# Kernel tuning notes

Measured on AMD Instinct MI355X. Metric: run time of the kernel, lower is better.

## Reference

```python
import jax, jax.numpy as jnp
import numpy as np

I = 1024
H = 1024
B = 4096
EPS = 1e-5

def layer_norm(x, gamma, beta):
    mu = jnp.mean(x, axis=-1, keepdims=True)
    var = jnp.var(x, axis=-1, keepdims=True)
    return (x - mu) * jax.lax.rsqrt(var + EPS) * gamma + beta

def setup_inputs() -> dict:
    key = jax.random.key(0)
    ks = jax.random.split(key, 5)
    return {
        "input": jax.random.normal(ks[0], (B, I), dtype=jnp.float32),
        "hx": jax.random.normal(ks[1], (B, H), dtype=jnp.float32),
        "cx": jax.random.normal(ks[2], (B, H), dtype=jnp.float32),
        "weight_ih": jax.random.normal(ks[3], (4 * H, I), dtype=jnp.float32),
        "weight_hh": jax.random.normal(ks[4], (4 * H, H), dtype=jnp.float32),
        "gamma_i": jnp.ones((4 * H,), jnp.float32),
        "beta_i": jnp.zeros((4 * H,), jnp.float32),
        "gamma_h": jnp.ones((4 * H,), jnp.float32),
        "beta_h": jnp.zeros((4 * H,), jnp.float32),
        "gamma_c": jnp.ones((H,), jnp.float32),
        "beta_c": jnp.zeros((H,), jnp.float32),
    }

def reference(input, hx, cx, weight_ih, weight_hh,
              gamma_i, beta_i, gamma_h, beta_h, gamma_c, beta_c):
    # igates: [B, 4H]
    igates = layer_norm(jnp.dot(input, weight_ih.T), gamma_i, beta_i)
    hgates = layer_norm(jnp.dot(hx, weight_hh.T), gamma_h, beta_h)
    gates = igates + hgates
    ingate, forgetgate, cellgate, outgate = jnp.split(gates, 4, axis=1)
    ingate = jax.nn.sigmoid(ingate)
    forgetgate = jax.nn.sigmoid(forgetgate)
    cellgate = jnp.tanh(cellgate)
    outgate = jax.nn.sigmoid(outgate)
    cy = layer_norm(forgetgate * cx + ingate * cellgate, gamma_c, beta_c)
    hy = outgate * jnp.tanh(cy)
    return (hy, hy, cy)
```

## Files before the change

kernel.cpp:

```cpp
#include <hip/hip_runtime.h>

#define EPS 1e-5f

typedef unsigned short u16;
typedef __attribute__((ext_vector_type(8))) __bf16 bf16x8;
typedef __attribute__((ext_vector_type(4))) float f32x4;
typedef __attribute__((ext_vector_type(8))) unsigned short ushort8;

__device__ inline float bf2f(u16 h) {
  union { unsigned u; float f; } x; x.u = ((unsigned)h) << 16; return x.f;
}
__device__ inline u16 f2bf(float f) {
  union { float f; unsigned u; } x; x.f = f;
  unsigned r = x.u + 0x7fffu + ((x.u >> 16) & 1u);
  return (u16)(r >> 16);
}
__device__ inline float sigmoidf(float x) { return 1.0f / (1.0f + __expf(-x)); }

__global__ __launch_bounds__(256) void cast4_f32_bf16(
    const float* __restrict__ s0, const float* __restrict__ s1,
    const float* __restrict__ s2, const float* __restrict__ s3,
    u16* __restrict__ d0, u16* __restrict__ d1,
    u16* __restrict__ d2, u16* __restrict__ d3, int n)
{
  const float* s = (blockIdx.y == 0) ? s0 : (blockIdx.y == 1) ? s1 : (blockIdx.y == 2) ? s2 : s3;
  u16*         d = (blockIdx.y == 0) ? d0 : (blockIdx.y == 1) ? d1 : (blockIdx.y == 2) ? d2 : d3;
  int i = (blockIdx.x * 256 + threadIdx.x) * 8;
  if (i >= n) return;
  float4 a = *(const float4*)(s + i);
  float4 b = *(const float4*)(s + i + 4);
  ushort8 o;
  o[0] = f2bf(a.x); o[1] = f2bf(a.y); o[2] = f2bf(a.z); o[3] = f2bf(a.w);
  o[4] = f2bf(b.x); o[5] = f2bf(b.y); o[6] = f2bf(b.z); o[7] = f2bf(b.w);
  *(ushort8*)(d + i) = o;
}

#define MFMA_ __builtin_amdgcn_mfma_f32_16x16x32_bf16

#define STAGE_A(nx, k0) { _Pragma("unroll") for (int i_ = 0; i_ < 4; ++i_) \
  __builtin_amdgcn_global_load_lds( \
      (const __attribute__((address_space(1))) void*)(gA + (size_t)(i_ * 64) * K + (k0)), \
      (__attribute__((address_space(3))) void*)(&sA[nx][(i_ * 512 + (w << 6)) * 8]), 16, 0, 0); }
#define STAGE_B(nx, k0) { _Pragma("unroll") for (int i_ = 0; i_ < 4; ++i_) \
  __builtin_amdgcn_global_load_lds( \
      (const __attribute__((address_space(1))) void*)(gB + (size_t)(i_ * 64) * K + (k0)), \
      (__attribute__((address_space(3))) void*)(&sB[nx][(i_ * 512 + (w << 6)) * 8]), 16, 0, 0); }

#define LDA(mi, sl) (*(const bf16x8*)&sa[(arow + (mi) * 16) * 64 + (sl)])
#define LDB(ni, sl) (*(const bf16x8*)&sb[(brow + (ni) * 16) * 64 + (sl)])

#define PHASE(m0, sl, RB) { \
  bf16x8 a0 = LDA(m0 + 0, sl), a1 = LDA(m0 + 1, sl), a2 = LDA(m0 + 2, sl), a3 = LDA(m0 + 3, sl); \
  if (RB) { q0 = LDB(0, sl); q1 = LDB(1, sl); q2 = LDB(2, sl); q3 = LDB(3, sl); } \
  __builtin_amdgcn_s_barrier(); \
  __builtin_amdgcn_s_setprio(1); \
  acc[m0 + 0][0] = MFMA_(a0, q0, acc[m0 + 0][0], 0, 0, 0); \
  acc[m0 + 0][1] = MFMA_(a0, q1, acc[m0 + 0][1], 0, 0, 0); \
  acc[m0 + 0][2] = MFMA_(a0, q2, acc[m0 + 0][2], 0, 0, 0); \
  acc[m0 + 0][3] = MFMA_(a0, q3, acc[m0 + 0][3], 0, 0, 0); \
  acc[m0 + 1][0] = MFMA_(a1, q0, acc[m0 + 1][0], 0, 0, 0); \
  acc[m0 + 1][1] = MFMA_(a1, q1, acc[m0 + 1][1], 0, 0, 0); \
  acc[m0 + 1][2] = MFMA_(a1, q2, acc[m0 + 1][2], 0, 0, 0); \
  acc[m0 + 1][3] = MFMA_(a1, q3, acc[m0 + 1][3], 0, 0, 0); \
  acc[m0 + 2][0] = MFMA_(a2, q0, acc[m0 + 2][0], 0, 0, 0); \
  acc[m0 + 2][1] = MFMA_(a2, q1, acc[m0 + 2][1], 0, 0, 0); \
  acc[m0 + 2][2] = MFMA_(a2, q2, acc[m0 + 2][2], 0, 0, 0); \
  acc[m0 + 2][3] = MFMA_(a2, q3, acc[m0 + 2][3], 0, 0, 0); \
  acc[m0 + 3][0] = MFMA_(a3, q0, acc[m0 + 3][0], 0, 0, 0); \
  acc[m0 + 3][1] = MFMA_(a3, q1, acc[m0 + 3][1], 0, 0, 0); \
  acc[m0 + 3][2] = MFMA_(a3, q2, acc[m0 + 3][2], 0, 0, 0); \
  acc[m0 + 3][3] = MFMA_(a3, q3, acc[m0 + 3][3], 0, 0, 0); \
  __builtin_amdgcn_s_setprio(0); }

__global__ __launch_bounds__(512, 2) void gemm256_dual(
    const u16* __restrict__ A0, const u16* __restrict__ W0, u16* __restrict__ C0,
    const u16* __restrict__ A1, const u16* __restrict__ W1, u16* __restrict__ C1)
{
  constexpr int K = 1024, N = 4096, NT = 16;

  __shared__ __attribute__((aligned(16))) u16 sA[2][256 * 64];
  __shared__ __attribute__((aligned(16))) u16 sB[2][256 * 64];

  const int bid = blockIdx.x;
  const u16* A  = (bid < 256) ? A0 : A1;
  const u16* Wm = (bid < 256) ? W0 : W1;
  u16*       C  = (bid < 256) ? C0 : C1;
  const int b2 = bid & 255;
  const int bm = (b2 >> 4) << 8;
  const int bn = (b2 & 15) << 8;

  const int tid = threadIdx.x;
  const int l  = tid & 63;
  const int w  = tid >> 6;
  const int wr = w >> 2;
  const int wc = w & 3;

  const int rb   = tid >> 3;
  const int slot = (tid & 7) ^ (rb & 7);
  const u16* gA = A  + (size_t)(bm + rb) * K + slot * 8;
  const u16* gB = Wm + (size_t)(bn + rb) * K + slot * 8;

  const int arow = wr * 128 + (l & 15);
  const int brow = wc * 64 + (l & 15);
  const int sl0 = (((l >> 4) + 0) ^ (l & 7)) * 8;
  const int sl1 = (((l >> 4) + 4) ^ (l & 7)) * 8;

  f32x4 acc[8][4];
#pragma unroll
  for (int i = 0; i < 8; ++i)
#pragma unroll
    for (int j = 0; j < 4; ++j) acc[i][j] = (f32x4){0.f, 0.f, 0.f, 0.f};

  STAGE_A(0, 0)
  STAGE_B(0, 0)
  __syncthreads();

  for (int t = 0; t < NT; ++t) {
    const int cur = t & 1, nxt = cur ^ 1;
    const int kn = (t + 1) << 6;
    const u16* sa = sA[cur];
    const u16* sb = sB[cur];
    bf16x8 q0, q1, q2, q3;

    if (t < NT - 1) STAGE_A(nxt, kn)
    PHASE(0, sl0, 1)
    __builtin_amdgcn_s_barrier();
    if (t < NT - 1) STAGE_B(nxt, kn)
    PHASE(4, sl0, 0)
    __builtin_amdgcn_s_barrier();
    PHASE(0, sl1, 1)
    __builtin_amdgcn_s_barrier();
    PHASE(4, sl1, 0)
    __syncthreads();
  }

  const int ccol = bn + wc * 64 + (l & 15);
  const int crow = bm + wr * 128 + (l >> 4) * 4;
#pragma unroll
  for (int mi = 0; mi < 8; ++mi) {
#pragma unroll
    for (int ni = 0; ni < 4; ++ni) {
      int col = ccol + ni * 16;
#pragma unroll
      for (int r = 0; r < 4; ++r) {
        int row = crow + mi * 16 + r;
        C[(size_t)row * N + col] = f2bf(acc[mi][ni][r]);
      }
    }
  }
}

__global__ __launch_bounds__(256) void lstm_epilogue(
    const u16* __restrict__ ig, const u16* __restrict__ hg,
    const float* __restrict__ cx,
    const float* __restrict__ gi, const float* __restrict__ bi,
    const float* __restrict__ gh, const float* __restrict__ bh,
    const float* __restrict__ gc, const float* __restrict__ bc,
    float* __restrict__ out)
{
  const int b = blockIdx.x;
  const int t = threadIdx.x;
  const u16* igr = ig + (size_t)b * 4096;
  const u16* hgr = hg + (size_t)b * 4096;

  __shared__ float redbuf[16];

  float iv[16], hv[16];
  float s_i = 0.f, q_i = 0.f, s_h = 0.f, q_h = 0.f;
#pragma unroll
  for (int i = 0; i < 16; ++i) {
    float a = bf2f(igr[t + 256 * i]);
    float c = bf2f(hgr[t + 256 * i]);
    iv[i] = a; hv[i] = c;
    s_i += a; q_i += a * a; s_h += c; q_h += c * c;
  }
#pragma unroll
  for (int off = 32; off > 0; off >>= 1) {
    s_i += __shfl_xor(s_i, off);
    q_i += __shfl_xor(q_i, off);
    s_h += __shfl_xor(s_h, off);
    q_h += __shfl_xor(q_h, off);
  }
  {
    int wv = t >> 6;
    if ((t & 63) == 0) {
      redbuf[wv] = s_i; redbuf[wv + 4] = q_i;
      redbuf[wv + 8] = s_h; redbuf[wv + 12] = q_h;
    }
    __syncthreads();
    s_i = redbuf[0] + redbuf[1] + redbuf[2] + redbuf[3];
    q_i = redbuf[4] + redbuf[5] + redbuf[6] + redbuf[7];
    s_h = redbuf[8] + redbuf[9] + redbuf[10] + redbuf[11];
    q_h = redbuf[12] + redbuf[13] + redbuf[14] + redbuf[15];
    __syncthreads();
  }
  const float inv4096 = 1.0f / 4096.0f;
  float mu_i = s_i * inv4096;
  float rs_i = rsqrtf(q_i * inv4096 - mu_i * mu_i + EPS);
  float mu_h = s_h * inv4096;
  float rs_h = rsqrtf(q_h * inv4096 - mu_h * mu_h + EPS);

  float c_pre[4], og[4];
  float s_c = 0.f, q_c = 0.f;
#pragma unroll
  for (int i = 0; i < 4; ++i) {
    int h = t + 256 * i;
    float g_in = ((iv[i]      - mu_i) * rs_i * gi[h]        + bi[h]) +
                 ((hv[i]      - mu_h) * rs_h * gh[h]        + bh[h]);
    float g_fg = ((iv[i + 4]  - mu_i) * rs_i * gi[h + 1024] + bi[h + 1024]) +
                 ((hv[i + 4]  - mu_h) * rs_h * gh[h + 1024] + bh[h + 1024]);
    float g_cl = ((iv[i + 8]  - mu_i) * rs_i * gi[h + 2048] + bi[h + 2048]) +
                 ((hv[i + 8]  - mu_h) * rs_h * gh[h + 2048] + bh[h + 2048]);
    float g_og = ((iv[i + 12] - mu_i) * rs_i * gi[h + 3072] + bi[h + 3072]) +
                 ((hv[i + 12] - mu_h) * rs_h * gh[h + 3072] + bh[h + 3072]);
    float in_s = sigmoidf(g_in);
    float fg_s = sigmoidf(g_fg);
    float cl_t = tanhf(g_cl);
    og[i] = sigmoidf(g_og);
    c_pre[i] = fg_s * cx[(size_t)b * 1024 + h] + in_s * cl_t;
    s_c += c_pre[i]; q_c += c_pre[i] * c_pre[i];
  }
#pragma unroll
  for (int off = 32; off > 0; off >>= 1) {
    s_c += __shfl_xor(s_c, off);
    q_c += __shfl_xor(q_c, off);
  }
  {
    int wv = t >> 6;
    if ((t & 63) == 0) { redbuf[wv] = s_c; redbuf[wv + 4] = q_c; }
    __syncthreads();
    s_c = redbuf[0] + redbuf[1] + redbuf[2] + redbuf[3];
    q_c = redbuf[4] + redbuf[5] + redbuf[6] + redbuf[7];
  }
  const float inv1024 = 1.0f / 1024.0f;
  float mu_c = s_c * inv1024;
  float rs_c = rsqrtf(q_c * inv1024 - mu_c * mu_c + EPS);

  const size_t BH = (size_t)4096 * 1024;
#pragma unroll
  for (int i = 0; i < 4; ++i) {
    int h = t + 256 * i;
    float cy = (c_pre[i] - mu_c) * rs_c * gc[h] + bc[h];
    float hy = og[i] * tanhf(cy);
    size_t o = (size_t)b * 1024 + h;
    out[o] = hy;
    out[BH + o] = hy;
    out[2 * BH + o] = cy;
  }
}

extern "C" void kernel_launch(void* const* d_in, const int* in_sizes, int n_in,
                              void* d_out, int out_size, void* d_ws, size_t ws_size,
                              hipStream_t stream) {
  const float* input = (const float*)d_in[0];
  const float* hx    = (const float*)d_in[1];
  const float* cx    = (const float*)d_in[2];
  const float* wih   = (const float*)d_in[3];
  const float* whh   = (const float*)d_in[4];
  const float* gi    = (const float*)d_in[5];
  const float* bi    = (const float*)d_in[6];
  const float* gh    = (const float*)d_in[7];
  const float* bh    = (const float*)d_in[8];
  const float* gc    = (const float*)d_in[9];
  const float* bc    = (const float*)d_in[10];
  float* out = (float*)d_out;

  char* wsp = (char*)d_ws;
  u16* a_bf  = (u16*)(wsp);
  u16* h_bf  = (u16*)(wsp + ((size_t)8  << 20));
  u16* wi_bf = (u16*)(wsp + ((size_t)16 << 20));
  u16* wh_bf = (u16*)(wsp + ((size_t)24 << 20));
  u16* ig_bf = (u16*)(wsp + ((size_t)32 << 20));
  u16* hg_bf = (u16*)(wsp + ((size_t)64 << 20));

  const int nper = 4096 * 1024;
  dim3 cgrid(nper / 8 / 256, 4);
  cast4_f32_bf16<<<cgrid, 256, 0, stream>>>(input, hx, wih, whh,
                                            a_bf, h_bf, wi_bf, wh_bf, nper);

  gemm256_dual<<<512, 512, 0, stream>>>(a_bf, wi_bf, ig_bf,
                                        h_bf, wh_bf, hg_bf);

  lstm_epilogue<<<4096, 256, 0, stream>>>(ig_bf, hg_bf, cx,
                                          gi, bi, gh, bh, gc, bc, out);
}
```

Before: 134.0 us.

## Restructure GEMM main loop with explicit vmcnt waits, fewer barriers, block swizzle

Rewrites the dual GEMM K-loop so that both A and B tiles for the next step are issued together, followed by an explicit s_waitcnt vmcnt(8) that waits only for the current tile's loads, and one barrier. Each half-K slice then does a single 12-fragment LDS read and 32 MFMAs, replacing the four phases with interleaved barriers. It also remaps block IDs so consecutive blocks spread across tiles, likely for L2/XCD locality, and precomputes per-row global pointers. The exchange is more live registers per thread and reliance on the hand-placed waitcnt to keep the LDS buffers correct.

```diff
diff --git a/kernel.cpp b/kernel.cpp
--- a/kernel.cpp
+++ b/kernel.cpp
@@ -36,41 +36,69 @@
 }
 
 #define MFMA_ __builtin_amdgcn_mfma_f32_16x16x32_bf16
-
-#define STAGE_A(nx, k0) { _Pragma("unroll") for (int i_ = 0; i_ < 4; ++i_) \
-  __builtin_amdgcn_global_load_lds( \
-      (const __attribute__((address_space(1))) void*)(gA + (size_t)(i_ * 64) * K + (k0)), \
-      (__attribute__((address_space(3))) void*)(&sA[nx][(i_ * 512 + (w << 6)) * 8]), 16, 0, 0); }
-#define STAGE_B(nx, k0) { _Pragma("unroll") for (int i_ = 0; i_ < 4; ++i_) \
-  __builtin_amdgcn_global_load_lds( \
-      (const __attribute__((address_space(1))) void*)(gB + (size_t)(i_ * 64) * K + (k0)), \
-      (__attribute__((address_space(3))) void*)(&sB[nx][(i_ * 512 + (w << 6)) * 8]), 16, 0, 0); }
+#define ASG __attribute__((address_space(1)))
+#define ASL __attribute__((address_space(3)))
+
+#define GLL(p, lds) __builtin_amdgcn_global_load_lds( \
+    (const ASG void*)(p), (ASL void*)(lds), 16, 0, 0);
+
+#define STAGE_A(nx, kn) \
+  GLL(gA_0 + (kn), &sA[nx][((w << 6)       ) * 8]) \
+  GLL(gA_1 + (kn), &sA[nx][((w << 6) +  512) * 8]) \
+  GLL(gA_2 + (kn), &sA[nx][((w << 6) + 1024) * 8]) \
+  GLL(gA_3 + (kn), &sA[nx][((w << 6) + 1536) * 8])
+#define STAGE_B(nx, kn) \
+  GLL(gB_0 + (kn), &sB[nx][((w << 6)       ) * 8]) \
+  GLL(gB_1 + (kn), &sB[nx][((w << 6) +  512) * 8]) \
+  GLL(gB_2 + (kn), &sB[nx][((w << 6) + 1024) * 8]) \
+  GLL(gB_3 + (kn), &sB[nx][((w << 6) + 1536) * 8])
 
 #define LDA(mi, sl) (*(const bf16x8*)&sa[(arow + (mi) * 16) * 64 + (sl)])
 #define LDB(ni, sl) (*(const bf16x8*)&sb[(brow + (ni) * 16) * 64 + (sl)])
 
-#define PHASE(m0, sl, RB) { \
-  bf16x8 a0 = LDA(m0 + 0, sl), a1 = LDA(m0 + 1, sl), a2 = LDA(m0 + 2, sl), a3 = LDA(m0 + 3, sl); \
-  if (RB) { q0 = LDB(0, sl); q1 = LDB(1, sl); q2 = LDB(2, sl); q3 = LDB(3, sl); } \
-  __builtin_amdgcn_s_barrier(); \
+#define VMW(n) asm volatile("s_waitcnt vmcnt(" #n ")" ::: "memory");
+#define BAR __builtin_amdgcn_s_barrier();
+
+#define MFMA32 \
   __builtin_amdgcn_s_setprio(1); \
-  acc[m0 + 0][0] = MFMA_(a0, q0, acc[m0 + 0][0], 0, 0, 0); \
-  acc[m0 + 0][1] = MFMA_(a0, q1, acc[m0 + 0][1], 0, 0, 0); \
-  acc[m0 + 0][2] = MFMA_(a0, q2, acc[m0 + 0][2], 0, 0, 0); \
-  acc[m0 + 0][3] = MFMA_(a0, q3, acc[m0 + 0][3], 0, 0, 0); \
-  acc[m0 + 1][0] = MFMA_(a1, q0, acc[m0 + 1][0], 0, 0, 0); \
-  acc[m0 + 1][1] = MFMA_(a1, q1, acc[m0 + 1][1], 0, 0, 0); \
-  acc[m0 + 1][2] = MFMA_(a1, q2, acc[m0 + 1][2], 0, 0, 0); \
-  acc[m0 + 1][3] = MFMA_(a1, q3, acc[m0 + 1][3], 0, 0, 0); \
-  acc[m0 + 2][0] = MFMA_(a2, q0, acc[m0 + 2][0], 0, 0, 0); \
-  acc[m0 + 2][1] = MFMA_(a2, q1, acc[m0 + 2][1], 0, 0, 0); \
-  acc[m0 + 2][2] = MFMA_(a2, q2, acc[m0 + 2][2], 0, 0, 0); \
-  acc[m0 + 2][3] = MFMA_(a2, q3, acc[m0 + 2][3], 0, 0, 0); \
-  acc[m0 + 3][0] = MFMA_(a3, q0, acc[m0 + 3][0], 0, 0, 0); \
-  acc[m0 + 3][1] = MFMA_(a3, q1, acc[m0 + 3][1], 0, 0, 0); \
-  acc[m0 + 3][2] = MFMA_(a3, q2, acc[m0 + 3][2], 0, 0, 0); \
-  acc[m0 + 3][3] = MFMA_(a3, q3, acc[m0 + 3][3], 0, 0, 0); \
-  __builtin_amdgcn_s_setprio(0); }
+  acc[0][0] = MFMA_(a0, b0, acc[0][0], 0, 0, 0); \
+  acc[0][1] = MFMA_(a0, b1, acc[0][1], 0, 0, 0); \
+  acc[0][2] = MFMA_(a0, b2, acc[0][2], 0, 0, 0); \
+  acc[0][3] = MFMA_(a0, b3, acc[0][3], 0, 0, 0); \
+  acc[1][0] = MFMA_(a1, b0, acc[1][0], 0, 0, 0); \
+  acc[1][1] = MFMA_(a1, b1, acc[1][1], 0, 0, 0); \
+  acc[1][2] = MFMA_(a1, b2, acc[1][2], 0, 0, 0); \
+  acc[1][3] = MFMA_(a1, b3, acc[1][3], 0, 0, 0); \
+  acc[2][0] = MFMA_(a2, b0, acc[2][0], 0, 0, 0); \
+  acc[2][1] = MFMA_(a2, b1, acc[2][1], 0, 0, 0); \
+  acc[2][2] = MFMA_(a2, b2, acc[2][2], 0, 0, 0); \
+  acc[2][3] = MFMA_(a2, b3, acc[2][3], 0, 0, 0); \
+  acc[3][0] = MFMA_(a3, b0, acc[3][0], 0, 0, 0); \
+  acc[3][1] = MFMA_(a3, b1, acc[3][1], 0, 0, 0); \
+  acc[3][2] = MFMA_(a3, b2, acc[3][2], 0, 0, 0); \
+  acc[3][3] = MFMA_(a3, b3, acc[3][3], 0, 0, 0); \
+  acc[4][0] = MFMA_(a4, b0, acc[4][0], 0, 0, 0); \
+  acc[4][1] = MFMA_(a4, b1, acc[4][1], 0, 0, 0); \
+  acc[4][2] = MFMA_(a4, b2, acc[4][2], 0, 0, 0); \
+  acc[4][3] = MFMA_(a4, b3, acc[4][3], 0, 0, 0); \
+  acc[5][0] = MFMA_(a5, b0, acc[5][0], 0, 0, 0); \
+  acc[5][1] = MFMA_(a5, b1, acc[5][1], 0, 0, 0); \
+  acc[5][2] = MFMA_(a5, b2, acc[5][2], 0, 0, 0); \
+  acc[5][3] = MFMA_(a5, b3, acc[5][3], 0, 0, 0); \
+  acc[6][0] = MFMA_(a6, b0, acc[6][0], 0, 0, 0); \
+  acc[6][1] = MFMA_(a6, b1, acc[6][1], 0, 0, 0); \
+  acc[6][2] = MFMA_(a6, b2, acc[6][2], 0, 0, 0); \
+  acc[6][3] = MFMA_(a6, b3, acc[6][3], 0, 0, 0); \
+  acc[7][0] = MFMA_(a7, b0, acc[7][0], 0, 0, 0); \
+  acc[7][1] = MFMA_(a7, b1, acc[7][1], 0, 0, 0); \
+  acc[7][2] = MFMA_(a7, b2, acc[7][2], 0, 0, 0); \
+  acc[7][3] = MFMA_(a7, b3, acc[7][3], 0, 0, 0); \
+  __builtin_amdgcn_s_setprio(0);
+
+#define RD12(sl) \
+  b0 = LDB(0, sl); b1 = LDB(1, sl); b2 = LDB(2, sl); b3 = LDB(3, sl); \
+  a0 = LDA(0, sl); a1 = LDA(1, sl); a2 = LDA(2, sl); a3 = LDA(3, sl); \
+  a4 = LDA(4, sl); a5 = LDA(5, sl); a6 = LDA(6, sl); a7 = LDA(7, sl);
 
 __global__ __launch_bounds__(512, 2) void gemm256_dual(
     const u16* __restrict__ A0, const u16* __restrict__ W0, u16* __restrict__ C0,
@@ -81,7 +109,9 @@
   __shared__ __attribute__((aligned(16))) u16 sA[2][256 * 64];
   __shared__ __attribute__((aligned(16))) u16 sB[2][256 * 64];
 
-  const int bid = blockIdx.x;
+  const int b0_ = blockIdx.x;
+  const int bid = (b0_ & 7) * 64 + (b0_ >> 3);
+
   const u16* A  = (bid < 256) ? A0 : A1;
   const u16* Wm = (bid < 256) ? W0 : W1;
   u16*       C  = (bid < 256) ? C0 : C1;
@@ -97,8 +127,14 @@
 
   const int rb   = tid >> 3;
   const int slot = (tid & 7) ^ (rb & 7);
-  const u16* gA = A  + (size_t)(bm + rb) * K + slot * 8;
-  const u16* gB = Wm + (size_t)(bn + rb) * K + slot * 8;
+  const u16* gA_0 = A  + (size_t)(bm + rb) * K + slot * 8;
+  const u16* gA_1 = gA_0 + (size_t)64  * K;
+  const u16* gA_2 = gA_0 + (size_t)128 * K;
+  const u16* gA_3 = gA_0 + (size_t)192 * K;
+  const u16* gB_0 = Wm + (size_t)(bn + rb) * K + slot * 8;
+  const u16* gB_1 = gB_0 + (size_t)64  * K;
+  const u16* gB_2 = gB_0 + (size_t)128 * K;
+  const u16* gB_3 = gB_0 + (size_t)192 * K;
 
   const int arow = wr * 128 + (l & 15);
   const int brow = wc * 64 + (l & 15);
@@ -113,25 +149,29 @@
 
   STAGE_A(0, 0)
   STAGE_B(0, 0)
-  __syncthreads();
 
   for (int t = 0; t < NT; ++t) {
     const int cur = t & 1, nxt = cur ^ 1;
-    const int kn = (t + 1) << 6;
     const u16* sa = sA[cur];
     const u16* sb = sB[cur];
-    bf16x8 q0, q1, q2, q3;
-
-    if (t < NT - 1) STAGE_A(nxt, kn)
-    PHASE(0, sl0, 1)
-    __builtin_amdgcn_s_barrier();
-    if (t < NT - 1) STAGE_B(nxt, kn)
-    PHASE(4, sl0, 0)
-    __builtin_amdgcn_s_barrier();
-    PHASE(0, sl1, 1)
-    __builtin_amdgcn_s_barrier();
-    PHASE(4, sl1, 0)
-    __syncthreads();
+
+    if (t < NT - 1) {
+      const int kn = (t + 1) << 6;
+      STAGE_A(nxt, kn)
+      STAGE_B(nxt, kn)
+      VMW(8)
+    } else {
+      VMW(0)
+    }
+    BAR
+
+    bf16x8 a0, a1, a2, a3, a4, a5, a6, a7, b0, b1, b2, b3;
+    RD12(sl0)
+    MFMA32
+    RD12(sl1)
+    MFMA32
+
+    BAR
   }
 
   const int ccol = bn + wc * 64 + (l & 15);
```

New measurement: 124.1 us (median of 2 runs). 7.4% less time.
